# Optimization experiments

Hardware: AMD Instinct MI355X
Metric: run time of the kernel (lower is better)

Reference implementation:

```python
import jax, jax.numpy as jnp
import numpy as np

D = 64        # inner_feature_len (dim)
HID = 128     # hidden_channels of the edge MLP
NCONV = 2     # n_conv
STEPS = 3     # Set2Set processing_steps
NSEG = 128    # number of graphs in the batch


def setup_inputs() -> dict:
    key = jax.random.key(0)
    ks = jax.random.split(key, 30)
    N, E, FN, FE = 10000, 64000, 92, 41
    s = 0.05
    p = lambda i, shape: jax.random.normal(ks[i], shape, jnp.float32) * s
    return {
        "x": jax.random.normal(ks[0], (N, FN), jnp.float32),
        "edge_attr": jax.random.uniform(ks[1], (E, FE), dtype=jnp.float32),
        "lin0_w": p(2, (D, FN)), "lin0_b": p(3, (D,)),
        "nn1_w": p(4, (HID, FE)), "nn1_b": p(5, (HID,)),
        "nn2_w": p(6, (D * D, HID)), "nn2_b": p(7, (D * D,)),
        "root_w": p(8, (D, D)), "conv_b": p(9, (D,)),
        "gru_w_ih": p(10, (3 * D, D)), "gru_w_hh": p(11, (3 * D, D)),
        "gru_b_ih": p(12, (3 * D,)), "gru_b_hh": p(13, (3 * D,)),
        "lstm_w_ih": p(14, (4 * D, 2 * D)), "lstm_w_hh": p(15, (4 * D, D)),
        "lstm_b_ih": p(16, (4 * D,)), "lstm_b_hh": p(17, (4 * D,)),
        "lin1_w": p(18, (D, 2 * D)), "lin1_b": p(19, (D,)),
        "lin2_w": p(20, (1, D)), "lin2_b": p(21, (1,)),
        "edge_index": jax.random.randint(ks[22], (2, E), 0, N, dtype=jnp.int32),
        "batch": jnp.sort(jax.random.randint(ks[23], (N,), 0, NSEG, dtype=jnp.int32)),
    }


def _gru_step(m, h, w_ih, w_hh, b_ih, b_hh):
    # torch GRU gate order: r, z, n
    gi = m @ w_ih.T + b_ih
    gh = h @ w_hh.T + b_hh
    r = jax.nn.sigmoid(gi[:, :D] + gh[:, :D])
    z = jax.nn.sigmoid(gi[:, D:2 * D] + gh[:, D:2 * D])
    n = jnp.tanh(gi[:, 2 * D:] + r * gh[:, 2 * D:])
    return (1.0 - z) * n + z * h


def _forward(x, edge_attr, lin0_w, lin0_b, nn1_w, nn1_b, nn2_w, nn2_b, root_w, conv_b,
             gru_w_ih, gru_w_hh, gru_b_ih, gru_b_hh, lstm_w_ih, lstm_w_hh, lstm_b_ih,
             lstm_b_hh, lin1_w, lin1_b, lin2_w, lin2_b, edge_index, batch):
    N = x.shape[0]
    src, dst = edge_index[0], edge_index[1]

    # Edge-conditioned weight matrices: [E, D, D] (dominant intermediate)
    We = (jax.nn.relu(edge_attr @ nn1_w.T + nn1_b) @ nn2_w.T + nn2_b).reshape(-1, D, D)
    deg = jnp.clip(jax.ops.segment_sum(jnp.ones_like(src, jnp.float32), dst, num_segments=N), 1.0, None)

    out = jax.nn.relu(x @ lin0_w.T + lin0_b)   # [N, D]
    h = out                                     # GRU hidden (num_layers=1)
    for _ in range(NCONV):
        # NNConv: gather -> per-edge matmul -> scatter-mean, plus root transform + bias
        msg = jnp.einsum('ei,eio->eo', out[src], We)                 # [E, D]
        agg = jax.ops.segment_sum(msg, dst, num_segments=N) / deg[:, None]
        m = jax.nn.relu(agg + out @ root_w.T + conv_b)
        h = _gru_step(m, h, gru_w_ih, gru_w_hh, gru_b_ih, gru_b_hh)
        out = h

    # Set2Set pooling (LSTM-attention readout)
    q_star = jnp.zeros((NSEG, 2 * D), x.dtype)
    hl = jnp.zeros((NSEG, D), x.dtype)
    cl = jnp.zeros((NSEG, D), x.dtype)
    for _ in range(STEPS):
        g = q_star @ lstm_w_ih.T + lstm_b_ih + hl @ lstm_w_hh.T + lstm_b_hh
        i = jax.nn.sigmoid(g[:, :D])
        f = jax.nn.sigmoid(g[:, D:2 * D])
        gg = jnp.tanh(g[:, 2 * D:3 * D])
        o = jax.nn.sigmoid(g[:, 3 * D:])
        cl = f * cl + i * gg
        hl = o * jnp.tanh(cl)
        q = hl                                   # [NSEG, D]
        e = jnp.sum(out * q[batch], axis=-1)     # [N]
        mmax = jax.ops.segment_max(e, batch, num_segments=NSEG)
        a = jnp.exp(e - mmax[batch])
        denom = jax.ops.segment_sum(a, batch, num_segments=NSEG)
        a = a / denom[batch]
        r = jax.ops.segment_sum(a[:, None] * out, batch, num_segments=NSEG)  # [NSEG, D]
        q_star = jnp.concatenate([q, r], axis=1)

    y = jax.nn.relu(q_star @ lin1_w.T + lin1_b) @ lin2_w.T + lin2_b
    return y.reshape(-1)


def reference(x, edge_attr, lin0_w, lin0_b, nn1_w, nn1_b, nn2_w, nn2_b, root_w, conv_b,
              gru_w_ih, gru_w_hh, gru_b_ih, gru_b_hh, lstm_w_ih, lstm_w_hh, lstm_b_ih,
              lstm_b_hh, lin1_w, lin1_b, lin2_w, lin2_b, edge_index, batch):
    return _forward(x, edge_attr, lin0_w, lin0_b, nn1_w, nn1_b, nn2_w, nn2_b, root_w,
                    conv_b, gru_w_ih, gru_w_hh, gru_b_ih, gru_b_hh, lstm_w_ih, lstm_w_hh,
                    lstm_b_ih, lstm_b_hh, lin1_w, lin1_b, lin2_w, lin2_b, edge_index, batch)
```

## Files before the change

kernel.cpp:

```cpp
#include <hip/hip_runtime.h>
#include <hip/hip_bf16.h>
#include <math.h>

#define DD 64
#define HIDC 128
#define FN 92
#define FE 41
#define S2CAP 192

typedef unsigned short u16;
typedef short bf16x8 __attribute__((ext_vector_type(8)));
typedef float f32x4 __attribute__((ext_vector_type(4)));
typedef u16 u16x8 __attribute__((ext_vector_type(8)));

__device__ __forceinline__ float sigmoidf_(float x){ return 1.f/(1.f+expf(-x)); }

__device__ __forceinline__ u16 f2bf(float v){
  union { float f; unsigned u; } x; x.f = v;
  unsigned r = x.u + 0x7fff + ((x.u >> 16) & 1);
  return (u16)(r >> 16);
}
__device__ __forceinline__ float bf2f(u16 v){
  union { float f; unsigned u; } x; x.u = ((unsigned)v) << 16;
  return x.f;
}
__device__ __forceinline__ void split_bf(float v, u16& h, u16& l){
  h = f2bf(v); l = f2bf(v - bf2f(h));
}

__global__ void k_pack(const float* __restrict__ lin0_w, const float* __restrict__ nn1_w,
                       const float* __restrict__ root_w, const float* __restrict__ gwih,
                       const float* __restrict__ gwhh, const float* __restrict__ lwih,
                       const float* __restrict__ lwhh, const float* __restrict__ lin1_w,
                       float* __restrict__ lin0T, float* __restrict__ nn1T,
                       float* __restrict__ rootT, float* __restrict__ wihT,
                       float* __restrict__ whhT, float* __restrict__ lwihT,
                       float* __restrict__ lwhhT, float* __restrict__ lin1T)
{
  int idx = blockIdx.x*blockDim.x + threadIdx.x;
  if (idx < 92*64){ int k=idx/64, o=idx%64; lin0T[k*64+o] = lin0_w[o*92+k]; return; } idx -= 92*64;
  if (idx < 41*128){ int k=idx/128, h=idx%128; nn1T[k*128+h] = nn1_w[h*41+k]; return; } idx -= 41*128;
  if (idx < 64*64){ int i=idx/64, o=idx%64; rootT[i*64+o] = root_w[o*64+i]; return; } idx -= 64*64;
  if (idx < 64*192){ int i=idx/192, g=idx%192; wihT[i*192+g] = gwih[g*64+i]; return; } idx -= 64*192;
  if (idx < 64*192){ int i=idx/192, g=idx%192; whhT[i*192+g] = gwhh[g*64+i]; return; } idx -= 64*192;
  if (idx < 128*256){ int j=idx/256, t=idx%256; lwihT[j*256+t] = lwih[t*128+j]; return; } idx -= 128*256;
  if (idx < 64*256){ int j=idx/256, t=idx%256; lwhhT[j*256+t] = lwhh[t*64+j]; return; } idx -= 64*256;
  if (idx < 128*64){ int j=idx/64, t=idx%64; lin1T[j*64+t] = lin1_w[t*128+j]; return; }
}

__global__ void k_pack_b2(const float* __restrict__ nn2_w,
                          u16* __restrict__ BhT, u16* __restrict__ BlT){
  int idx = blockIdx.x*256 + threadIdx.x;
  if (idx >= 524288) return;
  int i  = idx & 63;
  int ho = (idx >> 6) & 4095;
  int c  = idx >> 18;
  int h = ho >> 6, o = ho & 63;
  float v = nn2_w[(size_t)(i*64+o)*128 + c*64 + h];
  u16 hi, lo; split_bf(v, hi, lo);
  BhT[idx] = hi; BlT[idx] = lo;
}

__global__ void k_pack_b1(const float* __restrict__ nn1_w,
                          u16* __restrict__ BT1h, u16* __restrict__ BT1l){
  int idx = blockIdx.x*256 + threadIdx.x;
  if (idx >= 8192) return;
  int h = idx >> 6, k = idx & 63;
  float v = (k < FE) ? nn1_w[(size_t)h*FE + k] : 0.f;
  u16 hi, lo; split_bf(v, hi, lo);
  BT1h[idx] = hi; BT1l[idx] = lo;
}

__global__ void k_split_ea(const float* __restrict__ ea, const int* __restrict__ sortedE,
                           u16* __restrict__ eaH, u16* __restrict__ eaL, int E){
  int idx = blockIdx.x*256 + threadIdx.x;
  if (idx >= E*64) return;
  int ew = idx >> 6, k = idx & 63;
  int e = sortedE[ew];
  float v = (k < FE) ? ea[(size_t)e*FE + k] : 0.f;
  u16 hi, lo; split_bf(v, hi, lo);
  eaH[idx] = hi; eaL[idx] = lo;
}

__global__ __launch_bounds__(256) void k_node_mlp(const float* __restrict__ x,
    const float* __restrict__ lin0T, const float* __restrict__ lin0_b,
    const float* __restrict__ nn2_b,
    float* __restrict__ out, u16* __restrict__ outH, u16* __restrict__ outL,
    float* __restrict__ bterm, int N)
{
  __shared__ float xs[4][FN];
  int base = blockIdx.x*4;
  for (int i=threadIdx.x; i<4*FN; i+=256){
    int n = base + i/FN;
    xs[i/FN][i%FN] = (n<N) ? x[(size_t)n*FN + i%FN] : 0.f;
  }
  __syncthreads();
  int ln = threadIdx.x>>6, o = threadIdx.x&63;
  int n = base+ln;
  if (n>=N) return;
  float acc = lin0_b[o];
  #pragma unroll 4
  for (int k=0;k<FN;k++) acc = fmaf(xs[ln][k], lin0T[k*64+o], acc);
  float v = fmaxf(acc, 0.f);
  out[(size_t)n*64+o] = v;
  u16 hi, lo; split_bf(v, hi, lo);
  outH[(size_t)n*64+o] = hi;
  outL[(size_t)n*64+o] = lo;
  float bt = 0.f;
  #pragma unroll 8
  for (int i=0;i<64;i++) bt = fmaf(__shfl(v, i, 64), nn2_b[i*64+o], bt);
  bterm[(size_t)n*64+o] = bt;
}

__global__ void k_count(const int* __restrict__ dst, const int* __restrict__ src,
                        float* __restrict__ deg, int* __restrict__ scnt, int E){
  int e = blockIdx.x*blockDim.x + threadIdx.x;
  if (e < E){
    atomicAdd(&deg[dst[e]], 1.f);
    atomicAdd(&scnt[src[e]], 1);
  }
}

__global__ void k_scan1(const int* __restrict__ cnt, int* __restrict__ excl,
                        int* __restrict__ bsum, int N){
  __shared__ int buf[256];
  int i = blockIdx.x*256 + threadIdx.x;
  int v = (i<N) ? cnt[i] : 0;
  buf[threadIdx.x] = v;
  __syncthreads();
  #pragma unroll
  for (int off=1; off<256; off<<=1){
    int t = (threadIdx.x>=off) ? buf[threadIdx.x-off] : 0;
    __syncthreads();
    buf[threadIdx.x] += t;
    __syncthreads();
  }
  if (i<N) excl[i] = buf[threadIdx.x] - v;
  if (threadIdx.x==255) bsum[blockIdx.x] = buf[255];
}
__global__ void k_scan2(int* __restrict__ bsum, int nb){
  __shared__ int buf[256];
  int v = (threadIdx.x<nb) ? bsum[threadIdx.x] : 0;
  buf[threadIdx.x] = v;
  __syncthreads();
  #pragma unroll
  for (int off=1; off<256; off<<=1){
    int t = (threadIdx.x>=off) ? buf[threadIdx.x-off] : 0;
    __syncthreads();
    buf[threadIdx.x] += t;
    __syncthreads();
  }
  if (threadIdx.x<nb) bsum[threadIdx.x] = buf[threadIdx.x] - v;
}
__global__ void k_scan3(int* __restrict__ starts, int* __restrict__ cursor,
                        const int* __restrict__ bsum, int N, int E){
  int i = blockIdx.x*256 + threadIdx.x;
  if (i<N){
    int s = starts[i] + bsum[blockIdx.x];
    starts[i] = s;
    cursor[i] = s;
  }
  if (i==0) starts[N] = E;
}

__global__ void k_sort(const int* __restrict__ src, const int* __restrict__ dst,
                       int* __restrict__ cursor, int* __restrict__ sortedE,
                       int* __restrict__ dstS, int E){
  int e = blockIdx.x*256 + threadIdx.x;
  if (e < E){
    int s = src[e];
    int p = atomicAdd(&cursor[s], 1);
    sortedE[p] = e;
    dstS[p] = dst[e];
  }
}

__global__ __launch_bounds__(256,3) void k_edge_mlp_mfma(
    const u16* __restrict__ eaH, const u16* __restrict__ eaL,
    const u16* __restrict__ BT1h, const u16* __restrict__ BT1l,
    const float* __restrict__ nn1_b, float* __restrict__ hidden, int E)
{
  const int lane = threadIdx.x & 63;
  const int wave = threadIdx.x >> 6;
  const int row  = lane & 15;
  const int quad = lane >> 4;
  const int m0 = blockIdx.x*128 + (wave>>1)*64;
  const int n0 = (wave&1)*64;

  bf16x8 AH0[4], AH1[4], AL0[4], AL1[4];
  #pragma unroll
  for (int p=0;p<4;p++){
    int ar = min(m0 + p*16 + row, E-1);
    const u16* aH = eaH + (size_t)ar*64 + quad*8;
    const u16* aL = eaL + (size_t)ar*64 + quad*8;
    AH0[p] = *(const bf16x8*)(aH);
    AH1[p] = *(const bf16x8*)(aH + 32);
    AL0[p] = *(const bf16x8*)(aL);
    AL1[p] = *(const bf16x8*)(aL + 32);
  }
  #pragma unroll
  for (int tb=0;tb<4;tb++){
    const u16* bH = BT1h + (size_t)(n0 + tb*16 + row)*64 + quad*8;
    const u16* bL = BT1l + (size_t)(n0 + tb*16 + row)*64 + quad*8;
    bf16x8 bh0 = *(const bf16x8*)(bH);
    bf16x8 bh1 = *(const bf16x8*)(bH + 32);
    bf16x8 bl0 = *(const bf16x8*)(bL);
    bf16x8 bl1 = *(const bf16x8*)(bL + 32);
    float4 bias;
    {
      int nb = n0 + tb*16 + quad*4;
      bias.x = nn1_b[nb+0]; bias.y = nn1_b[nb+1];
      bias.z = nn1_b[nb+2]; bias.w = nn1_b[nb+3];
    }
    #pragma unroll
    for (int ta=0;ta<4;ta++){
      f32x4 a = {0.f,0.f,0.f,0.f};
      a = __builtin_amdgcn_mfma_f32_16x16x32_bf16(bh0, AH0[ta], a, 0,0,0);
      a = __builtin_amdgcn_mfma_f32_16x16x32_bf16(bh1, AH1[ta], a, 0,0,0);
      a = __builtin_amdgcn_mfma_f32_16x16x32_bf16(bl0, AH0[ta], a, 0,0,0);
      a = __builtin_amdgcn_mfma_f32_16x16x32_bf16(bl1, AH1[ta], a, 0,0,0);
      a = __builtin_amdgcn_mfma_f32_16x16x32_bf16(bh0, AL0[ta], a, 0,0,0);
      a = __builtin_amdgcn_mfma_f32_16x16x32_bf16(bh1, AL1[ta], a, 0,0,0);
      int m = m0 + ta*16 + row;
      if (m < E){
        float4 v;
        v.x = fmaxf(a[0]+bias.x, 0.f); v.y = fmaxf(a[1]+bias.y, 0.f);
        v.z = fmaxf(a[2]+bias.z, 0.f); v.w = fmaxf(a[3]+bias.w, 0.f);
        *(float4*)(hidden + (size_t)m*128 + n0 + tb*16 + quad*4) = v;
      }
    }
  }
}

__global__ __launch_bounds__(256,3) void k_qgemm_mfma(
    const u16* __restrict__ Ah, const u16* __restrict__ Al,
    const u16* __restrict__ BhT, const u16* __restrict__ BlT,
    u16* __restrict__ C, int M)
{
  const int lane = threadIdx.x & 63;
  const int wave = threadIdx.x >> 6;
  const int row  = lane & 15;
  const int quad = lane >> 4;
  const int m0 = blockIdx.y * 64;
  const int n0 = blockIdx.x * 256 + wave * 64;

  bf16x8 AH0[4], AH1[4], AL0[4], AL1[4];
  #pragma unroll
  for (int p=0;p<4;p++){
    int ar = min(m0 + p*16 + row, M-1);
    const u16* aH = Ah + (size_t)ar*64 + quad*8;
    const u16* aL = Al + (size_t)ar*64 + quad*8;
    AH0[p] = *(const bf16x8*)(aH);
    AH1[p] = *(const bf16x8*)(aH + 32);
    AL0[p] = *(const bf16x8*)(aL);
    AL1[p] = *(const bf16x8*)(aL + 32);
  }

  f32x4 acc[4][4];
  #pragma unroll
  for (int ta=0;ta<4;ta++)
    #pragma unroll
    for (int tb=0;tb<4;tb++)
      acc[ta][tb] = (f32x4){0.f,0.f,0.f,0.f};

  #pragma unroll
  for (int tb=0;tb<4;tb++){
    const u16* bH = BhT + (size_t)(n0 + tb*16 + row)*64 + quad*8;
    const u16* bL = BlT + (size_t)(n0 + tb*16 + row)*64 + quad*8;
    bf16x8 bh0 = *(const bf16x8*)(bH);
    bf16x8 bh1 = *(const bf16x8*)(bH + 32);
    bf16x8 bl0 = *(const bf16x8*)(bL);
    bf16x8 bl1 = *(const bf16x8*)(bL + 32);
    #pragma unroll
    for (int ta=0;ta<4;ta++){
      f32x4 a = acc[ta][tb];
      a = __builtin_amdgcn_mfma_f32_16x16x32_bf16(bh0, AH0[ta], a, 0,0,0);
      a = __builtin_amdgcn_mfma_f32_16x16x32_bf16(bh1, AH1[ta], a, 0,0,0);
      a = __builtin_amdgcn_mfma_f32_16x16x32_bf16(bl0, AH0[ta], a, 0,0,0);
      a = __builtin_amdgcn_mfma_f32_16x16x32_bf16(bl1, AH1[ta], a, 0,0,0);
      a = __builtin_amdgcn_mfma_f32_16x16x32_bf16(bh0, AL0[ta], a, 0,0,0);
      a = __builtin_amdgcn_mfma_f32_16x16x32_bf16(bh1, AL1[ta], a, 0,0,0);
      acc[ta][tb] = a;
    }
  }

  #pragma unroll
  for (int ta=0;ta<4;ta++){
    int m = m0 + ta*16 + row;
    if (m >= M) continue;
    u16* dst = C + (size_t)m*4096 + n0 + quad*8;
    #pragma unroll
    for (int p=0;p<2;p++){
      f32x4 aa = acc[ta][2*p];
      f32x4 ab = acc[ta][2*p+1];
      u16x8 v;
      v[0]=f2bf(aa[0]); v[1]=f2bf(aa[1]); v[2]=f2bf(aa[2]); v[3]=f2bf(aa[3]);
      v[4]=f2bf(ab[0]); v[5]=f2bf(ab[1]); v[6]=f2bf(ab[2]); v[7]=f2bf(ab[3]);
      *(u16x8*)(dst + p*32) = v;
    }
  }
}

template<int PASS>
__global__ __launch_bounds__(256) void k_edge_gather(const u16* __restrict__ Q,
    const float* __restrict__ hidden, int h0,
    const float* __restrict__ bterm, const int* __restrict__ starts,
    const int* __restrict__ dstS, float* __restrict__ agg, int N)
{
  __shared__ float hs[4][64];
  __shared__ float red[4][64];
  const int wv = threadIdx.x>>6, lane = threadIdx.x&63;
  const int n = blockIdx.x*4 + wv;
  if (n >= N) return;
  const int e0 = starts[n], e1 = starts[n+1];
  if (e0 >= e1) return;
  const int sg = lane>>4, oq = lane&15;
  const int posb = ((oq>>3)<<5) + ((oq&3)<<3) + (((oq>>2)&1)<<2);
  const u16* qp = Q + (size_t)n*4096 + sg*64 + posb;
  ushort4 qreg[16];
  #pragma unroll
  for (int j=0;j<16;j++) qreg[j] = *(const ushort4*)(qp + j*256);
  const float bt = (PASS==0) ? bterm[(size_t)n*64 + lane] : 0.f;

  float hvN = hidden[(size_t)e0*128 + h0 + lane];
  int   dN  = dstS[e0];
  for (int e=e0; e<e1; ++e){
    const float hv = hvN;
    const int   d  = dN;
    if (e+1 < e1){
      hvN = hidden[(size_t)(e+1)*128 + h0 + lane];
      dN  = dstS[e+1];
    }
    hs[wv][lane] = hv;
    float a0=0.f,a1=0.f,a2=0.f,a3=0.f;
    #pragma unroll
    for (int j=0;j<16;j++){
      float h4 = hs[wv][j*4+sg];
      a0 = fmaf(h4, bf2f(qreg[j].x), a0);
      a1 = fmaf(h4, bf2f(qreg[j].y), a1);
      a2 = fmaf(h4, bf2f(qreg[j].z), a2);
      a3 = fmaf(h4, bf2f(qreg[j].w), a3);
    }
    a0 += __shfl_xor(a0,16); a0 += __shfl_xor(a0,32);
    a1 += __shfl_xor(a1,16); a1 += __shfl_xor(a1,32);
    a2 += __shfl_xor(a2,16); a2 += __shfl_xor(a2,32);
    a3 += __shfl_xor(a3,16); a3 += __shfl_xor(a3,32);
    if (lane < 16){
      float4 r; r.x=a0; r.y=a1; r.z=a2; r.w=a3;
      *(float4*)&red[wv][lane*4] = r;
    }
    atomicAdd(&agg[(size_t)d*64 + lane], bt + red[wv][lane]);
  }
}

__global__ __launch_bounds__(256) void k_node_update(const float* __restrict__ outOld,
    const float* __restrict__ agg, const float* __restrict__ deg,
    const float* __restrict__ rootT, const float* __restrict__ conv_b,
    const float* __restrict__ wihT, const float* __restrict__ whhT,
    const float* __restrict__ b_ih, const float* __restrict__ b_hh,
    const float* __restrict__ nn2_b,
    float* __restrict__ outNew, u16* __restrict__ outH, u16* __restrict__ outL,
    float* __restrict__ bterm, int N)
{
  __shared__ float hs[4][64];
  __shared__ float ms[4][64];
  int ln = threadIdx.x>>6, o = threadIdx.x&63;
  int n = blockIdx.x*4+ln;
  bool ok = (n<N);
  float h = ok ? outOld[(size_t)n*64+o] : 0.f;
  hs[ln][o] = h;
  __syncthreads();
  float root = 0.f;
  #pragma unroll 8
  for (int i=0;i<64;i++) root = fmaf(hs[ln][i], rootT[i*64+o], root);
  float d = ok ? fmaxf(deg[n], 1.f) : 1.f;
  float a = ok ? agg[(size_t)n*64+o]/d : 0.f;
  float m = fmaxf(a + root + conv_b[o], 0.f);
  ms[ln][o] = m;
  __syncthreads();
  float gir=b_ih[o], giz=b_ih[64+o], gin=b_ih[128+o];
  float ghr=b_hh[o], ghz=b_hh[64+o], ghn=b_hh[128+o];
  #pragma unroll 4
  for (int i=0;i<64;i++){
    float mi = ms[ln][i], hi = hs[ln][i];
    gir = fmaf(mi, wihT[i*192+o],      gir);
    giz = fmaf(mi, wihT[i*192+64+o],   giz);
    gin = fmaf(mi, wihT[i*192+128+o],  gin);
    ghr = fmaf(hi, whhT[i*192+o],      ghr);
    ghz = fmaf(hi, whhT[i*192+64+o],   ghz);
    ghn = fmaf(hi, whhT[i*192+128+o],  ghn);
  }
  float r = sigmoidf_(gir+ghr);
  float z = sigmoidf_(giz+ghz);
  float nn = tanhf(gin + r*ghn);
  if (ok){
    float v = (1.f-z)*nn + z*h;
    outNew[(size_t)n*64+o] = v;
    u16 hi16, lo16; split_bf(v, hi16, lo16);
    outH[(size_t)n*64+o] = hi16;
    outL[(size_t)n*64+o] = lo16;
    float bt = 0.f;
    #pragma unroll 8
    for (int i=0;i<64;i++) bt = fmaf(__shfl(v, i, 64), nn2_b[i*64+o], bt);
    bterm[(size_t)n*64+o] = bt;
  }
}

__global__ __launch_bounds__(256) void k_set2set(const float* __restrict__ out,
    const int* __restrict__ batch, int N,
    const float* __restrict__ lwihT, const float* __restrict__ lwhhT,
    const float* __restrict__ b_ih, const float* __restrict__ b_hh,
    const float* __restrict__ lin1T, const float* __restrict__ lin1_b,
    const float* __restrict__ lin2_w, const float* __restrict__ lin2_b,
    float* __restrict__ y)
{
  __shared__ float X[S2CAP][65];
  __shared__ float earr[S2CAP];
  __shared__ float qstar[128], hl[64], cl[64], g[256];
  __shared__ float rpart[4][64], spart[4], redm[4], zs[64];
  __shared__ int sb[2];
  const int tid = threadIdx.x;
  const int b = blockIdx.x;
  const int wid = tid>>6, lane = tid&63;
  if (tid < 128) qstar[tid] = 0.f;
  if (tid < 64){ hl[tid]=0.f; cl[tid]=0.f; }
  if (tid == 0){
    int lo=0, hi=N;
    while (lo<hi){ int mid=(lo+hi)>>1; if (batch[mid] < b) lo=mid+1; else hi=mid; }
    sb[0]=lo;
    int lo2=lo, hi2=N;
    while (lo2<hi2){ int mid=(lo2+hi2)>>1; if (batch[mid] < b+1) lo2=mid+1; else hi2=mid; }
    sb[1]=lo2;
  }
  __syncthreads();
  const int nlo = sb[0], nhi = sb[1], nn = nhi - nlo;
  const bool single = (nn <= S2CAP);
  if (single){
    for (int idx = tid; idx < nn*64; idx += 256){
      X[idx>>6][idx&63] = out[(size_t)(nlo + (idx>>6))*64 + (idx&63)];
    }
  }
  __syncthreads();

  for (int step=0; step<3; step++){
    float gs = b_ih[tid] + b_hh[tid];
    for (int j=0;j<128;j++) gs = fmaf(qstar[j], lwihT[j*256+tid], gs);
    for (int j=0;j<64;j++)  gs = fmaf(hl[j],    lwhhT[j*256+tid], gs);
    g[tid] = gs;
    __syncthreads();
    if (tid < 64){
      float ig = sigmoidf_(g[tid]);
      float fg = sigmoidf_(g[64+tid]);
      float gg = tanhf(g[128+tid]);
      float og = sigmoidf_(g[192+tid]);
      float c = fg*cl[tid] + ig*gg;
      cl[tid] = c;
      hl[tid] = og*tanhf(c);
    }
    __syncthreads();

    if (single){
      float lm = -INFINITY;
      for (int n = tid; n < nn; n += 256){
        float acc = 0.f;
        #pragma unroll 8
        for (int d=0; d<64; d++) acc = fmaf(X[n][d], hl[d], acc);
        earr[n] = acc;
        lm = fmaxf(lm, acc);
      }
      lm = fmaxf(lm, __shfl_xor(lm,1));  lm = fmaxf(lm, __shfl_xor(lm,2));
      lm = fmaxf(lm, __shfl_xor(lm,4));  lm = fmaxf(lm, __shfl_xor(lm,8));
      lm = fmaxf(lm, __shfl_xor(lm,16)); lm = fmaxf(lm, __shfl_xor(lm,32));
      if (lane==0) redm[wid] = lm;
      __syncthreads();
      if (tid==0) redm[0] = fmaxf(fmaxf(redm[0],redm[1]), fmaxf(redm[2],redm[3]));
      __syncthreads();
      const float gmax = redm[0];
      float ls = 0.f;
      for (int n = tid; n < nn; n += 256){
        float a = expf(earr[n] - gmax);
        earr[n] = a;
        ls += a;
      }
      ls += __shfl_xor(ls,1);  ls += __shfl_xor(ls,2);  ls += __shfl_xor(ls,4);
      ls += __shfl_xor(ls,8);  ls += __shfl_xor(ls,16); ls += __shfl_xor(ls,32);
      if (lane==0) spart[wid] = ls;
      __syncthreads();
      float racc = 0.f;
      for (int n = wid; n < nn; n += 4) racc = fmaf(earr[n], X[n][lane], racc);
      rpart[wid][lane] = racc;
      __syncthreads();
      if (tid < 64){
        float r = rpart[0][tid]+rpart[1][tid]+rpart[2][tid]+rpart[3][tid];
        float s = spart[0]+spart[1]+spart[2]+spart[3];
        qstar[tid] = hl[tid];
        qstar[64+tid] = (nn>0) ? r/s : 0.f;
      }
      __syncthreads();
    } else {
      float qv = hl[lane];
      float lm = -INFINITY;
      for (int n = nlo + wid; n < nhi; n += 4){
        float p = out[(size_t)n*64 + lane]*qv;
        p += __shfl_xor(p,1); p += __shfl_xor(p,2); p += __shfl_xor(p,4);
        p += __shfl_xor(p,8); p += __shfl_xor(p,16); p += __shfl_xor(p,32);
        lm = fmaxf(lm, p);
      }
      if (lane==0) redm[wid] = lm;
      __syncthreads();
      if (tid==0) redm[0] = fmaxf(fmaxf(redm[0],redm[1]), fmaxf(redm[2],redm[3]));
      __syncthreads();
      float gmax = redm[0];
      float sw = 0.f, racc = 0.f;
      for (int n = nlo + wid; n < nhi; n += 4){
        float ol = out[(size_t)n*64 + lane];
        float p = ol*qv;
        p += __shfl_xor(p,1); p += __shfl_xor(p,2); p += __shfl_xor(p,4);
        p += __shfl_xor(p,8); p += __shfl_xor(p,16); p += __shfl_xor(p,32);
        float a = expf(p - gmax);
        sw += a;
        racc = fmaf(a, ol, racc);
      }
      rpart[wid][lane] = racc;
      if (lane==0) spart[wid] = sw;
      __syncthreads();
      if (tid < 64){
        float r = rpart[0][tid]+rpart[1][tid]+rpart[2][tid]+rpart[3][tid];
        float s = spart[0]+spart[1]+spart[2]+spart[3];
        qstar[tid] = hl[tid];
        qstar[64+tid] = (nn>0) ? r/s : 0.f;
      }
      __syncthreads();
    }
  }
  if (tid < 64){
    float acc = lin1_b[tid];
    for (int j=0;j<128;j++) acc = fmaf(qstar[j], lin1T[j*64+tid], acc);
    zs[tid] = fmaxf(acc, 0.f);
  }
  __syncthreads();
  if (tid < 64){
    float v = zs[lane]*lin2_w[lane];
    v += __shfl_xor(v,1); v += __shfl_xor(v,2); v += __shfl_xor(v,4);
    v += __shfl_xor(v,8); v += __shfl_xor(v,16); v += __shfl_xor(v,32);
    if (lane==0) y[b] = v + lin2_b[0];
  }
}

extern "C" void kernel_launch(void* const* d_in, const int* in_sizes, int n_in,
                              void* d_out, int out_size, void* d_ws, size_t ws_size,
                              hipStream_t stream)
{
  const float* x      = (const float*)d_in[0];
  const float* eattr  = (const float*)d_in[1];
  const float* lin0_w = (const float*)d_in[2];
  const float* lin0_b = (const float*)d_in[3];
  const float* nn1_w  = (const float*)d_in[4];
  const float* nn1_b  = (const float*)d_in[5];
  const float* nn2_w  = (const float*)d_in[6];
  const float* nn2_b  = (const float*)d_in[7];
  const float* root_w = (const float*)d_in[8];
  const float* conv_b = (const float*)d_in[9];
  const float* gwih   = (const float*)d_in[10];
  const float* gwhh   = (const float*)d_in[11];
  const float* gbih   = (const float*)d_in[12];
  const float* gbhh   = (const float*)d_in[13];
  const float* lwih   = (const float*)d_in[14];
  const float* lwhh   = (const float*)d_in[15];
  const float* lbih   = (const float*)d_in[16];
  const float* lbhh   = (const float*)d_in[17];
  const float* lin1_w = (const float*)d_in[18];
  const float* lin1_b = (const float*)d_in[19];
  const float* lin2_w = (const float*)d_in[20];
  const float* lin2_b = (const float*)d_in[21];
  const int*   eidx   = (const int*)d_in[22];
  const int*   batch  = (const int*)d_in[23];

  const int N = in_sizes[0]/FN;
  const int E = in_sizes[1]/FE;
  const int* srcI = eidx;
  const int* dstI = eidx + E;

  char* w = (char*)d_ws;
  size_t off = 0;
  auto alloc = [&](size_t bytes)->char* {
    char* p = w + off;
    off = (off + bytes + 255) & ~(size_t)255;
    return p;
  };
  float* degw  = (float*)alloc((size_t)N*4);
  int*   scnt  = (int*)alloc((size_t)N*4);
  int*   starts= (int*)alloc((size_t)(N+1)*4);
  int*   cursor= (int*)alloc((size_t)N*4);
  int*   bsum  = (int*)alloc((size_t)256*4);
  int*   sortedE=(int*)alloc((size_t)E*4);
  int*   dstS  = (int*)alloc((size_t)E*4);
  float* outA  = (float*)alloc((size_t)N*64*4);
  float* outB  = (float*)alloc((size_t)N*64*4);
  u16*   outAH = (u16*)alloc((size_t)N*64*2);
  u16*   outAL = (u16*)alloc((size_t)N*64*2);
  u16*   outBH = (u16*)alloc((size_t)N*64*2);
  u16*   outBL = (u16*)alloc((size_t)N*64*2);
  float* agg   = (float*)alloc((size_t)N*64*4);
  float* bterm = (float*)alloc((size_t)N*64*4);
  float* hidden= (float*)alloc((size_t)E*128*4);
  u16*   B2hT  = (u16*)alloc((size_t)524288*2);
  u16*   B2lT  = (u16*)alloc((size_t)524288*2);
  u16*   BT1h  = (u16*)alloc((size_t)8192*2);
  u16*   BT1l  = (u16*)alloc((size_t)8192*2);
  float* lin0T = (float*)alloc((size_t)92*64*4);
  float* nn1T  = (float*)alloc((size_t)41*128*4);
  float* rootT = (float*)alloc((size_t)64*64*4);
  float* wihT  = (float*)alloc((size_t)64*192*4);
  float* whhT  = (float*)alloc((size_t)64*192*4);
  float* lwihT = (float*)alloc((size_t)128*256*4);
  float* lwhhT = (float*)alloc((size_t)64*256*4);
  float* lin1T = (float*)alloc((size_t)128*64*4);
  u16*   Q     = (u16*)alloc((size_t)N*4096*2);
  u16* eaH = (u16*)Q;
  u16* eaL = eaH + (size_t)E*64;

  const int NB = (N+255)/256;

  hipMemsetAsync(degw, 0, (size_t)N*4, stream);
  hipMemsetAsync(scnt, 0, (size_t)N*4, stream);
  k_pack<<<(97152+255)/256, 256, 0, stream>>>(lin0_w, nn1_w, root_w, gwih, gwhh,
      lwih, lwhh, lin1_w, lin0T, nn1T, rootT, wihT, whhT, lwihT, lwhhT, lin1T);
  k_pack_b2<<<524288/256, 256, 0, stream>>>(nn2_w, B2hT, B2lT);
  k_pack_b1<<<8192/256, 256, 0, stream>>>(nn1_w, BT1h, BT1l);
  k_node_mlp<<<(N+3)/4, 256, 0, stream>>>(x, lin0T, lin0_b, nn2_b, outA, outAH, outAL, bterm, N);
  k_count<<<(E+255)/256, 256, 0, stream>>>(dstI, srcI, degw, scnt, E);
  k_scan1<<<NB, 256, 0, stream>>>(scnt, starts, bsum, N);
  k_scan2<<<1, 256, 0, stream>>>(bsum, NB);
  k_scan3<<<NB, 256, 0, stream>>>(starts, cursor, bsum, N, E);
  k_sort<<<(E+255)/256, 256, 0, stream>>>(srcI, dstI, cursor, sortedE, dstS, E);
  k_split_ea<<<((size_t)E*64+255)/256, 256, 0, stream>>>(eattr, sortedE, eaH, eaL, E);
  k_edge_mlp_mfma<<<(E+127)/128, 256, 0, stream>>>(eaH, eaL, BT1h, BT1l, nn1_b, hidden, E);

  float* cur = outA; float* nxt = outB;
  u16* curH = outAH; u16* curL = outAL;
  u16* nxtH = outBH; u16* nxtL = outBL;
  const dim3 qgrid(16, (N+63)/64);
  const int gatherG = (N+3)/4;
  for (int conv=0; conv<2; conv++){
    hipMemsetAsync(agg, 0, (size_t)N*64*4, stream);
    k_qgemm_mfma<<<qgrid, 256, 0, stream>>>(curH, curL, B2hT, B2lT, Q, N);
    k_edge_gather<0><<<gatherG, 256, 0, stream>>>(Q, hidden, 0, bterm, starts, dstS, agg, N);
    k_qgemm_mfma<<<qgrid, 256, 0, stream>>>(curH, curL, B2hT + 262144, B2lT + 262144, Q, N);
    k_edge_gather<1><<<gatherG, 256, 0, stream>>>(Q, hidden, 64, bterm, starts, dstS, agg, N);
    k_node_update<<<(N+3)/4, 256, 0, stream>>>(cur, agg, degw, rootT, conv_b,
        wihT, whhT, gbih, gbhh, nn2_b, nxt, nxtH, nxtL, bterm, N);
    float* t = cur; cur = nxt; nxt = t;
    u16* th = curH; curH = nxtH; nxtH = th;
    u16* tl = curL; curL = nxtL; nxtL = tl;
  }

  k_set2set<<<128, 256, 0, stream>>>(cur, batch, N, lwihT, lwhhT, lbih, lbhh,
      lin1T, lin1_b, lin2_w, lin2_b, (float*)d_out);
}
```

Before: 573.4 us.

## Merge hidden-half Q GEMM and gather passes, batch 4 nodes per wave

When the workspace is large enough, the two half-width Q GEMM plus edge-gather passes are merged into one GEMM writing an 8192-wide Q and one gather that processes all 128 hidden channels per edge. This halves the number of edge traversals and launches. The gather now broadcasts hidden values through shuffles instead of shared memory. The node MLP and node-update kernels now process 4 nodes per wave, so each weight load is reused four times. In exchange, the gather holds twice as many Q registers (risking occupancy), and the Q buffer doubles in size.

```diff
diff --git a/kernel.cpp b/kernel.cpp
--- a/kernel.cpp
+++ b/kernel.cpp
@@ -88,28 +88,46 @@
     float* __restrict__ out, u16* __restrict__ outH, u16* __restrict__ outL,
     float* __restrict__ bterm, int N)
 {
-  __shared__ float xs[4][FN];
-  int base = blockIdx.x*4;
-  for (int i=threadIdx.x; i<4*FN; i+=256){
-    int n = base + i/FN;
-    xs[i/FN][i%FN] = (n<N) ? x[(size_t)n*FN + i%FN] : 0.f;
-  }
-  __syncthreads();
-  int ln = threadIdx.x>>6, o = threadIdx.x&63;
-  int n = base+ln;
-  if (n>=N) return;
-  float acc = lin0_b[o];
-  #pragma unroll 4
-  for (int k=0;k<FN;k++) acc = fmaf(xs[ln][k], lin0T[k*64+o], acc);
-  float v = fmaxf(acc, 0.f);
-  out[(size_t)n*64+o] = v;
-  u16 hi, lo; split_bf(v, hi, lo);
-  outH[(size_t)n*64+o] = hi;
-  outL[(size_t)n*64+o] = lo;
-  float bt = 0.f;
-  #pragma unroll 8
-  for (int i=0;i<64;i++) bt = fmaf(__shfl(v, i, 64), nn2_b[i*64+o], bt);
-  bterm[(size_t)n*64+o] = bt;
+  __shared__ float xs[16][FN];
+  const int w = threadIdx.x>>6, o = threadIdx.x&63;
+  const int nb = blockIdx.x*16 + w*4;
+  for (int idx = o; idx < 4*FN; idx += 64){
+    int j = idx/FN, k = idx%FN;
+    int n = nb + j;
+    xs[w*4+j][k] = (n<N) ? x[(size_t)n*FN + k] : 0.f;
+  }
+  float acc[4];
+  float bv = lin0_b[o];
+  #pragma unroll
+  for (int j=0;j<4;j++) acc[j] = bv;
+  for (int k=0;k<FN;k++){
+    float lw = lin0T[k*64+o];
+    #pragma unroll
+    for (int j=0;j<4;j++) acc[j] = fmaf(xs[w*4+j][k], lw, acc[j]);
+  }
+  float v[4];
+  #pragma unroll
+  for (int j=0;j<4;j++){
+    v[j] = fmaxf(acc[j], 0.f);
+    int n = nb + j;
+    if (n < N){
+      out[(size_t)n*64+o] = v[j];
+      u16 hi, lo; split_bf(v[j], hi, lo);
+      outH[(size_t)n*64+o] = hi;
+      outL[(size_t)n*64+o] = lo;
+    }
+  }
+  float bt[4] = {0.f,0.f,0.f,0.f};
+  for (int i=0;i<64;i++){
+    float wnb = nn2_b[i*64+o];
+    #pragma unroll
+    for (int j=0;j<4;j++) bt[j] = fmaf(__shfl(v[j], i, 64), wnb, bt[j]);
+  }
+  #pragma unroll
+  for (int j=0;j<4;j++){
+    int n = nb + j;
+    if (n < N) bterm[(size_t)n*64+o] = bt[j];
+  }
 }
 
 __global__ void k_count(const int* __restrict__ dst, const int* __restrict__ src,
@@ -235,14 +253,18 @@
 __global__ __launch_bounds__(256,3) void k_qgemm_mfma(
     const u16* __restrict__ Ah, const u16* __restrict__ Al,
     const u16* __restrict__ BhT, const u16* __restrict__ BlT,
-    u16* __restrict__ C, int M)
+    u16* __restrict__ C, int M, int QS, int cbase)
 {
   const int lane = threadIdx.x & 63;
   const int wave = threadIdx.x >> 6;
   const int row  = lane & 15;
   const int quad = lane >> 4;
   const int m0 = blockIdx.y * 64;
-  const int n0 = blockIdx.x * 256 + wave * 64;
+  const int col = cbase + blockIdx.x * 256 + wave * 64;
+  const int chunk = col >> 12;
+  const int n0 = col & 4095;
+  const u16* Bh = BhT + (size_t)chunk*262144;
+  const u16* Bl = BlT + (size_t)chunk*262144;
 
   bf16x8 AH0[4], AH1[4], AL0[4], AL1[4];
   #pragma unroll
@@ -265,8 +287,8 @@
 
   #pragma unroll
   for (int tb=0;tb<4;tb++){
-    const u16* bH = BhT + (size_t)(n0 + tb*16 + row)*64 + quad*8;
-    const u16* bL = BlT + (size_t)(n0 + tb*16 + row)*64 + quad*8;
+    const u16* bH = Bh + (size_t)(n0 + tb*16 + row)*64 + quad*8;
+    const u16* bL = Bl + (size_t)(n0 + tb*16 + row)*64 + quad*8;
     bf16x8 bh0 = *(const bf16x8*)(bH);
     bf16x8 bh1 = *(const bf16x8*)(bH + 32);
     bf16x8 bl0 = *(const bf16x8*)(bL);
@@ -288,7 +310,7 @@
   for (int ta=0;ta<4;ta++){
     int m = m0 + ta*16 + row;
     if (m >= M) continue;
-    u16* dst = C + (size_t)m*4096 + n0 + quad*8;
+    u16* dst = C + (size_t)m*QS + (col - cbase) + quad*8;
     #pragma unroll
     for (int p=0;p<2;p++){
       f32x4 aa = acc[ta][2*p];
@@ -301,13 +323,14 @@
   }
 }
 
-template<int PASS>
+template<int NH>
 __global__ __launch_bounds__(256) void k_edge_gather(const u16* __restrict__ Q,
-    const float* __restrict__ hidden, int h0,
+    const float* __restrict__ hidden, int h0, int addbt,
     const float* __restrict__ bterm, const int* __restrict__ starts,
     const int* __restrict__ dstS, float* __restrict__ agg, int N)
 {
-  __shared__ float hs[4][64];
+  constexpr int NJ = NH/4;
+  constexpr int QS = NH*64;
   __shared__ float red[4][64];
   const int wv = threadIdx.x>>6, lane = threadIdx.x&63;
   const int n = blockIdx.x*4 + wv;
@@ -316,26 +339,27 @@
   if (e0 >= e1) return;
   const int sg = lane>>4, oq = lane&15;
   const int posb = ((oq>>3)<<5) + ((oq&3)<<3) + (((oq>>2)&1)<<2);
-  const u16* qp = Q + (size_t)n*4096 + sg*64 + posb;
-  ushort4 qreg[16];
-  #pragma unroll
-  for (int j=0;j<16;j++) qreg[j] = *(const ushort4*)(qp + j*256);
-  const float bt = (PASS==0) ? bterm[(size_t)n*64 + lane] : 0.f;
-
-  float hvN = hidden[(size_t)e0*128 + h0 + lane];
-  int   dN  = dstS[e0];
+  const u16* qp = Q + (size_t)n*QS + sg*64 + posb;
+  ushort4 qreg[NJ];
+  #pragma unroll
+  for (int j=0;j<NJ;j++) qreg[j] = *(const ushort4*)(qp + (size_t)j*256);
+  const float bt = addbt ? bterm[(size_t)n*64 + lane] : 0.f;
+
+  float hA = hidden[(size_t)e0*128 + h0 + lane];
+  float hB = (NH==128) ? hidden[(size_t)e0*128 + h0 + 64 + lane] : 0.f;
+  int dN = dstS[e0];
   for (int e=e0; e<e1; ++e){
-    const float hv = hvN;
-    const int   d  = dN;
+    const float h0v = hA, h1v = hB;
+    const int d = dN;
     if (e+1 < e1){
-      hvN = hidden[(size_t)(e+1)*128 + h0 + lane];
-      dN  = dstS[e+1];
-    }
-    hs[wv][lane] = hv;
+      hA = hidden[(size_t)(e+1)*128 + h0 + lane];
+      if (NH==128) hB = hidden[(size_t)(e+1)*128 + h0 + 64 + lane];
+      dN = dstS[e+1];
+    }
     float a0=0.f,a1=0.f,a2=0.f,a3=0.f;
     #pragma unroll
-    for (int j=0;j<16;j++){
-      float h4 = hs[wv][j*4+sg];
+    for (int j=0;j<NJ;j++){
+      float h4 = __shfl((j<16) ? h0v : h1v, ((j*4)&63)+sg, 64);
       a0 = fmaf(h4, bf2f(qreg[j].x), a0);
       a1 = fmaf(h4, bf2f(qreg[j].y), a1);
       a2 = fmaf(h4, bf2f(qreg[j].z), a2);
@@ -362,47 +386,76 @@
     float* __restrict__ outNew, u16* __restrict__ outH, u16* __restrict__ outL,
     float* __restrict__ bterm, int N)
 {
-  __shared__ float hs[4][64];
-  __shared__ float ms[4][64];
-  int ln = threadIdx.x>>6, o = threadIdx.x&63;
-  int n = blockIdx.x*4+ln;
-  bool ok = (n<N);
-  float h = ok ? outOld[(size_t)n*64+o] : 0.f;
-  hs[ln][o] = h;
-  __syncthreads();
-  float root = 0.f;
-  #pragma unroll 8
-  for (int i=0;i<64;i++) root = fmaf(hs[ln][i], rootT[i*64+o], root);
-  float d = ok ? fmaxf(deg[n], 1.f) : 1.f;
-  float a = ok ? agg[(size_t)n*64+o]/d : 0.f;
-  float m = fmaxf(a + root + conv_b[o], 0.f);
-  ms[ln][o] = m;
-  __syncthreads();
-  float gir=b_ih[o], giz=b_ih[64+o], gin=b_ih[128+o];
-  float ghr=b_hh[o], ghz=b_hh[64+o], ghn=b_hh[128+o];
-  #pragma unroll 4
+  __shared__ float hs[16][64];
+  __shared__ float ms[16][64];
+  const int w = threadIdx.x>>6, o = threadIdx.x&63;
+  const int nb = blockIdx.x*16 + w*4;
+  float h[4];
+  #pragma unroll
+  for (int j=0;j<4;j++){
+    int n = nb+j;
+    h[j] = (n<N) ? outOld[(size_t)n*64+o] : 0.f;
+    hs[w*4+j][o] = h[j];
+  }
+  float root[4] = {0.f,0.f,0.f,0.f};
   for (int i=0;i<64;i++){
-    float mi = ms[ln][i], hi = hs[ln][i];
-    gir = fmaf(mi, wihT[i*192+o],      gir);
-    giz = fmaf(mi, wihT[i*192+64+o],   giz);
-    gin = fmaf(mi, wihT[i*192+128+o],  gin);
-    ghr = fmaf(hi, whhT[i*192+o],      ghr);
-    ghz = fmaf(hi, whhT[i*192+64+o],   ghz);
-    ghn = fmaf(hi, whhT[i*192+128+o],  ghn);
-  }
-  float r = sigmoidf_(gir+ghr);
-  float z = sigmoidf_(giz+ghz);
-  float nn = tanhf(gin + r*ghn);
-  if (ok){
-    float v = (1.f-z)*nn + z*h;
-    outNew[(size_t)n*64+o] = v;
-    u16 hi16, lo16; split_bf(v, hi16, lo16);
-    outH[(size_t)n*64+o] = hi16;
-    outL[(size_t)n*64+o] = lo16;
-    float bt = 0.f;
-    #pragma unroll 8
-    for (int i=0;i<64;i++) bt = fmaf(__shfl(v, i, 64), nn2_b[i*64+o], bt);
-    bterm[(size_t)n*64+o] = bt;
+    float rw = rootT[i*64+o];
+    #pragma unroll
+    for (int j=0;j<4;j++) root[j] = fmaf(hs[w*4+j][i], rw, root[j]);
+  }
+  float cb = conv_b[o];
+  float m[4];
+  #pragma unroll
+  for (int j=0;j<4;j++){
+    int n = nb+j;
+    float d = (n<N) ? fmaxf(deg[n], 1.f) : 1.f;
+    float a = (n<N) ? agg[(size_t)n*64+o]/d : 0.f;
+    m[j] = fmaxf(a + root[j] + cb, 0.f);
+    ms[w*4+j][o] = m[j];
+  }
+  float gir[4],giz[4],gin[4],ghr[4],ghz[4],ghn[4];
+  float bir=b_ih[o], biz=b_ih[64+o], bin=b_ih[128+o];
+  float bhr=b_hh[o], bhz=b_hh[64+o], bhn=b_hh[128+o];
+  #pragma unroll
+  for (int j=0;j<4;j++){
+    gir[j]=bir; giz[j]=biz; gin[j]=bin;
+    ghr[j]=bhr; ghz[j]=bhz; ghn[j]=bhn;
+  }
+  for (int i=0;i<64;i++){
+    float wr=wihT[i*192+o], wz=wihT[i*192+64+o], wn=wihT[i*192+128+o];
+    float vr=whhT[i*192+o], vz=whhT[i*192+64+o], vn=whhT[i*192+128+o];
+    #pragma unroll
+    for (int j=0;j<4;j++){
+      float mi = ms[w*4+j][i], hi = hs[w*4+j][i];
+      gir[j]=fmaf(mi,wr,gir[j]); giz[j]=fmaf(mi,wz,giz[j]); gin[j]=fmaf(mi,wn,gin[j]);
+      ghr[j]=fmaf(hi,vr,ghr[j]); ghz[j]=fmaf(hi,vz,ghz[j]); ghn[j]=fmaf(hi,vn,ghn[j]);
+    }
+  }
+  float v[4];
+  #pragma unroll
+  for (int j=0;j<4;j++){
+    float r = sigmoidf_(gir[j]+ghr[j]);
+    float z = sigmoidf_(giz[j]+ghz[j]);
+    float nn = tanhf(gin[j] + r*ghn[j]);
+    v[j] = (1.f-z)*nn + z*h[j];
+    int n = nb+j;
+    if (n<N){
+      outNew[(size_t)n*64+o] = v[j];
+      u16 hi16, lo16; split_bf(v[j], hi16, lo16);
+      outH[(size_t)n*64+o] = hi16;
+      outL[(size_t)n*64+o] = lo16;
+    }
+  }
+  float bt[4] = {0.f,0.f,0.f,0.f};
+  for (int i=0;i<64;i++){
+    float wnb = nn2_b[i*64+o];
+    #pragma unroll
+    for (int j=0;j<4;j++) bt[j] = fmaf(__shfl(v[j], i, 64), wnb, bt[j]);
+  }
+  #pragma unroll
+  for (int j=0;j<4;j++){
+    int n = nb+j;
+    if (n<N) bterm[(size_t)n*64+o] = bt[j];
   }
 }
 
@@ -616,7 +669,11 @@
   float* lwihT = (float*)alloc((size_t)128*256*4);
   float* lwhhT = (float*)alloc((size_t)64*256*4);
   float* lin1T = (float*)alloc((size_t)128*64*4);
-  u16*   Q     = (u16*)alloc((size_t)N*4096*2);
+
+  size_t qbig = (size_t)N*8192*2;
+  size_t qsmall = (size_t)N*4096*2;
+  bool merged = (ws_size - off) >= (qbig + 512);
+  u16* Q = (u16*)alloc(merged ? qbig : qsmall);
   u16* eaH = (u16*)Q;
   u16* eaL = eaH + (size_t)E*64;
 
@@ -628,7 +685,7 @@
       lwih, lwhh, lin1_w, lin0T, nn1T, rootT, wihT, whhT, lwihT, lwhhT, lin1T);
   k_pack_b2<<<524288/256, 256, 0, stream>>>(nn2_w, B2hT, B2lT);
   k_pack_b1<<<8192/256, 256, 0, stream>>>(nn1_w, BT1h, BT1l);
-  k_node_mlp<<<(N+3)/4, 256, 0, stream>>>(x, lin0T, lin0_b, nn2_b, outA, outAH, outAL, bterm, N);
+  k_node_mlp<<<(N+15)/16, 256, 0, stream>>>(x, lin0T, lin0_b, nn2_b, outA, outAH, outAL, bterm, N);
   k_count<<<(E+255)/256, 256, 0, stream>>>(dstI, srcI, degw, scnt, E);
   k_scan1<<<NB, 256, 0, stream>>>(scnt, starts, bsum, N);
   k_scan2<<<1, 256, 0, stream>>>(bsum, NB);
@@ -640,15 +697,19 @@
   float* cur = outA; float* nxt = outB;
   u16* curH = outAH; u16* curL = outAL;
   u16* nxtH = outBH; u16* nxtL = outBL;
-  const dim3 qgrid(16, (N+63)/64);
   const int gatherG = (N+3)/4;
   for (int conv=0; conv<2; conv++){
     hipMemsetAsync(agg, 0, (size_t)N*64*4, stream);
-    k_qgemm_mfma<<<qgrid, 256, 0, stream>>>(curH, curL, B2hT, B2lT, Q, N);
-    k_edge_gather<0><<<gatherG, 256, 0, stream>>>(Q, hidden, 0, bterm, starts, dstS, agg, N);
-    k_qgemm_mfma<<<qgrid, 256, 0, stream>>>(curH, curL, B2hT + 262144, B2lT + 262144, Q, N);
-    k_edge_gather<1><<<gatherG, 256, 0, stream>>>(Q, hidden, 64, bterm, starts, dstS, agg, N);
-    k_node_update<<<(N+3)/4, 256, 0, stream>>>(cur, agg, degw, rootT, conv_b,
+    if (merged){
+      k_qgemm_mfma<<<dim3(32,(N+63)/64), 256, 0, stream>>>(curH, curL, B2hT, B2lT, Q, N, 8192, 0);
+      k_edge_gather<128><<<gatherG, 256, 0, stream>>>(Q, hidden, 0, 1, bterm, starts, dstS, agg, N);
+    } else {
+      for (int c=0; c<2; c++){
+        k_qgemm_mfma<<<dim3(16,(N+63)/64), 256, 0, stream>>>(curH, curL, B2hT, B2lT, Q, N, 4096, c*4096);
+        k_edge_gather<64><<<gatherG, 256, 0, stream>>>(Q, hidden, c*64, (c==0)?1:0, bterm, starts, dstS, agg, N);
+      }
+    }
+    k_node_update<<<(N+15)/16, 256, 0, stream>>>(cur, agg, degw, rootT, conv_b,
         wihT, whhT, gbih, gbhh, nn2_b, nxt, nxtH, nxtL, bterm, N);
     float* t = cur; cur = nxt; nxt = t;
     u16* th = curH; curH = nxtH; nxtH = th;
```

Result: slower. 601.9 us (+5.0%).
